# Kernel optimization log

Hardware: AMD Instinct MI355X
Metric: run time of the kernel (lower is better)

Reference implementation:

```python
import jax, jax.numpy as jnp
import numpy as np


def setup_inputs() -> dict:
    key = jax.random.key(0)
    tensor = jax.random.normal(key, (1024, 32768), dtype=jnp.float32)
    return {"tensor": tensor}


def reference(tensor):
    # Fused equivalent of the per-channel Python loop: for each channel
    # (leading dim), compute min and max over all remaining elements.
    C = tensor.shape[0]
    flat = tensor.reshape(C, -1)  # [C, N]
    min_vals = jnp.min(flat, axis=1)  # [C]
    max_vals = jnp.max(flat, axis=1)  # [C]
    return min_vals, max_vals
```

## Files before the change

kernel.cpp:

```cpp
#include <hip/hip_runtime.h>
#include <math.h>


#define BS 1024

template <int PER>
__global__ __launch_bounds__(BS) void cw_minmax_spec(
    const float* __restrict__ in, float* __restrict__ out, int nvec, int C) {
    const int c = blockIdx.x;
    const float4* __restrict__ row =
        reinterpret_cast<const float4*>(in) + (size_t)c * nvec;

    float4 v[PER];
    #pragma unroll
    for (int k = 0; k < PER; ++k)
        v[k] = row[threadIdx.x + k * BS];

    float vmin = INFINITY, vmax = -INFINITY;
    #pragma unroll
    for (int k = 0; k < PER; ++k) {
        vmin = fminf(vmin, fminf(fminf(v[k].x, v[k].y), fminf(v[k].z, v[k].w)));
        vmax = fmaxf(vmax, fmaxf(fmaxf(v[k].x, v[k].y), fmaxf(v[k].z, v[k].w)));
    }

    #pragma unroll
    for (int off = 32; off > 0; off >>= 1) {
        vmin = fminf(vmin, __shfl_xor(vmin, off, 64));
        vmax = fmaxf(vmax, __shfl_xor(vmax, off, 64));
    }

    __shared__ float smin[BS / 64];
    __shared__ float smax[BS / 64];
    const int wave = threadIdx.x >> 6;
    const int lane = threadIdx.x & 63;
    if (lane == 0) { smin[wave] = vmin; smax[wave] = vmax; }
    __syncthreads();

    if (threadIdx.x == 0) {
        float m = smin[0], M = smax[0];
        #pragma unroll
        for (int w = 1; w < BS / 64; ++w) {
            m = fminf(m, smin[w]);
            M = fmaxf(M, smax[w]);
        }
        out[c] = m;
        out[C + c] = M;
    }
}

__global__ __launch_bounds__(256) void cw_minmax_generic(
    const float* __restrict__ in, float* __restrict__ out, int N, int C) {
    const int c = blockIdx.x;
    const float* __restrict__ row = in + (size_t)c * N;

    float vmin = INFINITY, vmax = -INFINITY;
    for (int i = threadIdx.x; i < N; i += blockDim.x) {
        float x = row[i];
        vmin = fminf(vmin, x);
        vmax = fmaxf(vmax, x);
    }
    #pragma unroll
    for (int off = 32; off > 0; off >>= 1) {
        vmin = fminf(vmin, __shfl_xor(vmin, off, 64));
        vmax = fmaxf(vmax, __shfl_xor(vmax, off, 64));
    }
    __shared__ float smin[4];
    __shared__ float smax[4];
    const int wave = threadIdx.x >> 6;
    const int lane = threadIdx.x & 63;
    if (lane == 0) { smin[wave] = vmin; smax[wave] = vmax; }
    __syncthreads();
    if (threadIdx.x == 0) {
        float m = smin[0], M = smax[0];
        for (int w = 1; w < 4; ++w) {
            m = fminf(m, smin[w]);
            M = fmaxf(M, smax[w]);
        }
        out[c] = m;
        out[C + c] = M;
    }
}

extern "C" void kernel_launch(void* const* d_in, const int* in_sizes, int n_in,
                              void* d_out, int out_size, void* d_ws, size_t ws_size,
                              hipStream_t stream) {
    const float* in = (const float*)d_in[0];
    float* out = (float*)d_out;

    const int C = out_size / 2;
    const int N = in_sizes[0] / C;

    if (N % (4 * BS) == 0) {
        const int nvec = N / 4;
        const int per = nvec / BS;
        switch (per) {
            case 4:  cw_minmax_spec<4><<<C, BS, 0, stream>>>(in, out, nvec, C);  return;
            case 8:  cw_minmax_spec<8><<<C, BS, 0, stream>>>(in, out, nvec, C);  return;
            case 16: cw_minmax_spec<16><<<C, BS, 0, stream>>>(in, out, nvec, C); return;
            default: break;
        }
    }
    cw_minmax_generic<<<C, 256, 0, stream>>>(in, out, N, C);
}
```

Measured before the change: 183.5 us.

## Split each channel row across multiple blocks with a two-pass min/max reduction

Replaces the one-block-per-channel reduction with a split: many 256-thread blocks each reduce a 4096-float segment into a workspace of partial min/max values, and a second small kernel combines the partials per channel. The aim is to raise the number of independent blocks and memory requests in flight and to shorten per-block tails, for more memory-bandwidth parallelism. The cost is an extra kernel launch, a workspace round trip, and a dependence on the workspace being present and large enough. The old path remains as a fallback.

```diff
diff --git a/kernel.cpp b/kernel.cpp
--- a/kernel.cpp
+++ b/kernel.cpp
@@ -2,7 +2,73 @@
 #include <math.h>
 
 
+#define BS2 256
 #define BS 1024
+
+template <int PER>
+__global__ __launch_bounds__(BS2) void cw_minmax_part(
+    const float* __restrict__ in, float* __restrict__ part,
+    int nvec, int segs) {
+    const int c   = blockIdx.x / segs;
+    const int seg = blockIdx.x % segs;
+    const float4* __restrict__ p =
+        reinterpret_cast<const float4*>(in) + (size_t)c * nvec
+        + (size_t)seg * (BS2 * PER);
+
+    float4 v[PER];
+    #pragma unroll
+    for (int k = 0; k < PER; ++k)
+        v[k] = p[threadIdx.x + k * BS2];
+
+    float vmin = INFINITY, vmax = -INFINITY;
+    #pragma unroll
+    for (int k = 0; k < PER; ++k) {
+        vmin = fminf(vmin, fminf(fminf(v[k].x, v[k].y), fminf(v[k].z, v[k].w)));
+        vmax = fmaxf(vmax, fmaxf(fmaxf(v[k].x, v[k].y), fmaxf(v[k].z, v[k].w)));
+    }
+
+    #pragma unroll
+    for (int off = 32; off > 0; off >>= 1) {
+        vmin = fminf(vmin, __shfl_xor(vmin, off, 64));
+        vmax = fmaxf(vmax, __shfl_xor(vmax, off, 64));
+    }
+
+    __shared__ float smin[BS2 / 64];
+    __shared__ float smax[BS2 / 64];
+    const int wave = threadIdx.x >> 6;
+    const int lane = threadIdx.x & 63;
+    if (lane == 0) { smin[wave] = vmin; smax[wave] = vmax; }
+    __syncthreads();
+
+    if (threadIdx.x == 0) {
+        float m = smin[0], M = smax[0];
+        #pragma unroll
+        for (int w = 1; w < BS2 / 64; ++w) {
+            m = fminf(m, smin[w]);
+            M = fmaxf(M, smax[w]);
+        }
+        const int ntot = gridDim.x;
+        part[blockIdx.x] = m;
+        part[ntot + blockIdx.x] = M;
+    }
+}
+
+__global__ __launch_bounds__(BS2) void cw_minmax_fin(
+    const float* __restrict__ part, float* __restrict__ out, int C, int segs) {
+    const int t = blockIdx.x * BS2 + threadIdx.x;
+    if (t >= 2 * C) return;
+    const bool isMax = (t >= C);
+    const int row = isMax ? t - C : t;
+    const float* __restrict__ p =
+        part + (isMax ? (size_t)C * segs : (size_t)0) + (size_t)row * segs;
+    float r = p[0];
+    if (isMax) {
+        for (int s = 1; s < segs; ++s) r = fmaxf(r, p[s]);
+    } else {
+        for (int s = 1; s < segs; ++s) r = fminf(r, p[s]);
+    }
+    out[t] = r;
+}
 
 template <int PER>
 __global__ __launch_bounds__(BS) void cw_minmax_spec(
@@ -22,20 +88,17 @@
         vmin = fminf(vmin, fminf(fminf(v[k].x, v[k].y), fminf(v[k].z, v[k].w)));
         vmax = fmaxf(vmax, fmaxf(fmaxf(v[k].x, v[k].y), fmaxf(v[k].z, v[k].w)));
     }
-
     #pragma unroll
     for (int off = 32; off > 0; off >>= 1) {
         vmin = fminf(vmin, __shfl_xor(vmin, off, 64));
         vmax = fmaxf(vmax, __shfl_xor(vmax, off, 64));
     }
-
     __shared__ float smin[BS / 64];
     __shared__ float smax[BS / 64];
     const int wave = threadIdx.x >> 6;
     const int lane = threadIdx.x & 63;
     if (lane == 0) { smin[wave] = vmin; smax[wave] = vmax; }
     __syncthreads();
-
     if (threadIdx.x == 0) {
         float m = smin[0], M = smax[0];
         #pragma unroll
@@ -90,14 +153,28 @@
     const int C = out_size / 2;
     const int N = in_sizes[0] / C;
 
-    if (N % (4 * BS) == 0) {
+    if (N % 4 == 0) {
         const int nvec = N / 4;
-        const int per = nvec / BS;
-        switch (per) {
-            case 4:  cw_minmax_spec<4><<<C, BS, 0, stream>>>(in, out, nvec, C);  return;
-            case 8:  cw_minmax_spec<8><<<C, BS, 0, stream>>>(in, out, nvec, C);  return;
-            case 16: cw_minmax_spec<16><<<C, BS, 0, stream>>>(in, out, nvec, C); return;
-            default: break;
+        constexpr int PER = 4;
+        if (nvec % (BS2 * PER) == 0) {
+            const int segs = nvec / (BS2 * PER);
+            const size_t need = (size_t)2 * C * segs * sizeof(float);
+            if (d_ws != nullptr && ws_size >= need && segs >= 1) {
+                float* part = (float*)d_ws;
+                cw_minmax_part<PER><<<C * segs, BS2, 0, stream>>>(in, part, nvec, segs);
+                const int fin_blocks = (2 * C + BS2 - 1) / BS2;
+                cw_minmax_fin<<<fin_blocks, BS2, 0, stream>>>(part, out, C, segs);
+                return;
+            }
+        }
+        if (nvec % BS == 0) {
+            const int per = nvec / BS;
+            switch (per) {
+                case 4:  cw_minmax_spec<4><<<C, BS, 0, stream>>>(in, out, nvec, C);  return;
+                case 8:  cw_minmax_spec<8><<<C, BS, 0, stream>>>(in, out, nvec, C);  return;
+                case 16: cw_minmax_spec<16><<<C, BS, 0, stream>>>(in, out, nvec, C); return;
+                default: break;
+            }
         }
     }
     cw_minmax_generic<<<C, 256, 0, stream>>>(in, out, N, C);
```

After: 184.4 us. About the same (+0.5%).
